# Optimization experiments

Hardware: AMD Instinct MI355X
Metric: run time of the kernel (lower is better)

Reference implementation:

```python
import jax, jax.numpy as jnp
import numpy as np

B, C, H, W = 16, 1024, 64, 64  # H*W must equal 64*64=4096 per module math
KDIM = 64

def setup_inputs() -> dict:
    key = jax.random.key(0)
    k1, k2 = jax.random.split(key)
    x = jax.random.normal(k1, (B, C, H, W), dtype=jnp.float32)
    martx = jax.random.normal(k2, (1, H * W, KDIM), dtype=jnp.float32) * 0.02
    aphal = jnp.ones((1,), dtype=jnp.float32)
    gamma = jnp.ones((1,), dtype=jnp.float32)
    return {"x": x, "martx": martx, "aphal": aphal, "gamma": gamma}

def reference(x, martx, aphal, gamma):
    b, c, h, w = x.shape
    n = h * w  # 4096
    q = x.reshape(b, c, n)                      # proj_query: (B, C, N)
    kbank = martx[0]                            # (N, 64), shared across batch
    # energy = bmm(q, martx): (B, C, 64)
    energy = jnp.einsum('bcn,nk->bck', q, kbank)
    # inverted max-subtract trick, then scaled softmax over last dim
    energy_new = jnp.max(energy, axis=-1, keepdims=True) - energy
    attention = jax.nn.softmax(aphal[0] * energy_new, axis=-1)  # (B, C, 64)
    # out = bmm(attention, martx^T): (B, C, N)
    out = jnp.einsum('bck,nk->bcn', attention, kbank)
    out = out.reshape(b, c, h, w)
    return gamma[0] * out + x
```

## Files before the change

kernel.cpp:

```cpp
#include <hip/hip_runtime.h>
#include <hip/hip_bf16.h>


using frag_ab = __attribute__((ext_vector_type(8))) short;
using f32x4   = __attribute__((ext_vector_type(4))) float;

#define MFMA16(a, b, c) __builtin_amdgcn_mfma_f32_16x16x32_bf16((a), (b), (c), 0, 0, 0)

static __device__ __forceinline__ unsigned short f2bf_bits(float f) {
    __hip_bfloat16 h = __float2bfloat16(f);
    return *reinterpret_cast<const unsigned short*>(&h);
}
static __device__ __forceinline__ float bf2f(unsigned short u) {
    return __uint_as_float(((unsigned)u) << 16);
}
static __device__ __forceinline__ frag_ab load_frag(const __hip_bfloat16* p) {
    return *reinterpret_cast<const frag_ab*>(p);
}
static __device__ __forceinline__ frag_ab cvt2(float4 a, float4 b) {
    frag_ab r;
    r[0] = (short)f2bf_bits(a.x); r[1] = (short)f2bf_bits(a.y);
    r[2] = (short)f2bf_bits(a.z); r[3] = (short)f2bf_bits(a.w);
    r[4] = (short)f2bf_bits(b.x); r[5] = (short)f2bf_bits(b.y);
    r[6] = (short)f2bf_bits(b.z); r[7] = (short)f2bf_bits(b.w);
    return r;
}

__global__ __launch_bounds__(256) void prep_frags(
        const float* __restrict__ M,
        __hip_bfloat16* __restrict__ MtF, __hip_bfloat16* __restrict__ MbfF) {
    const int w    = threadIdx.x >> 6;
    const int lane = threadIdx.x & 63;
    const int g    = lane >> 4;
    const int r15  = lane & 15;
    const int f    = blockIdx.x * 4 + w;
    if (f < 512) {
        const int slot = f >> 2, t = f & 3;
        frag_ab fr;
#pragma unroll
        for (int j = 0; j < 8; ++j)
            fr[j] = (short)f2bf_bits(M[(size_t)(32 * slot + 8 * g + j) * 64 + 16 * t + r15]);
        *reinterpret_cast<frag_ab*>(MtF + ((size_t)f * 64 + lane) * 8) = fr;
    } else {
        const int f2 = f - 512;
        const float* src = M + (size_t)(16 * (f2 >> 1) + r15) * 64 + 32 * (f2 & 1) + 8 * g;
        float4 a = *reinterpret_cast<const float4*>(src);
        float4 b = *reinterpret_cast<const float4*>(src + 4);
        *reinterpret_cast<frag_ab*>(MbfF + ((size_t)f2 * 64 + lane) * 8) = cvt2(a, b);
    }
}

__global__ __launch_bounds__(1024, 1) void ccam_fused(
        const float* __restrict__ x,
        const __hip_bfloat16* __restrict__ MtF,
        const __hip_bfloat16* __restrict__ MbfF,
        const float* __restrict__ aphal,
        const float* __restrict__ gamma,
        float* __restrict__ out) {
    __shared__ __align__(16) char smem[147712];
    float* Ep = (float*)(smem + 131328);

    const int tid  = threadIdx.x;
    const int w    = tid >> 6;
    const int lane = tid & 63;
    const int g    = lane >> 4;
    const int r15  = lane & 15;
    const int rowbase = blockIdx.x * 16;

    const float alpha = aphal[0];
    const float gam   = gamma[0];

    {
        const float* xr = x + (size_t)(rowbase + w) * 4096;
        char* dst = smem + w * 8208;
#pragma unroll
        for (int rnd = 0; rnd < 2; ++rnd) {
            f32x4 v[8];
#pragma unroll
            for (int i = 0; i < 8; ++i)
                v[i] = __builtin_nontemporal_load(
                    reinterpret_cast<const f32x4*>(xr + rnd * 2048 + i * 256 + 4 * lane));
#pragma unroll
            for (int i = 0; i < 8; ++i) {
                ushort4 u;
                u.x = f2bf_bits(v[i][0]); u.y = f2bf_bits(v[i][1]);
                u.z = f2bf_bits(v[i][2]); u.w = f2bf_bits(v[i][3]);
                *reinterpret_cast<ushort4*>(dst + (rnd * 2048 + i * 256 + 4 * lane) * 2) = u;
            }
        }
    }
    __syncthreads();

    const int t1 = w >> 2;
    const int kq = w & 3;
    {
        f32x4 acc = {0.f, 0.f, 0.f, 0.f};
        const char* arow = smem + r15 * 8208;
        const int kbase = kq * 1024;
        const int slot0 = kq * 32;
        frag_ab Bc = load_frag(MtF + (((size_t)slot0 * 4 + t1) * 64 + lane) * 8);
        frag_ab Bn = load_frag(MtF + (((size_t)(slot0 + 1) * 4 + t1) * 64 + lane) * 8);
#pragma unroll 4
        for (int s = 0; s < 32; ++s) {
            frag_ab Bn2 = Bn;
            if (s < 30)
                Bn2 = load_frag(MtF + (((size_t)(slot0 + s + 2) * 4 + t1) * 64 + lane) * 8);
            frag_ab A = *reinterpret_cast<const frag_ab*>(
                arow + (kbase + 32 * s + 8 * g) * 2);
            acc = MFMA16(A, Bc, acc);
            Bc = Bn;
            Bn = Bn2;
        }
#pragma unroll
        for (int reg = 0; reg < 4; ++reg)
            Ep[(((t1 * 4 + kq) * 16) + 4 * g + reg) * 16 + r15] = acc[reg];
    }
    __syncthreads();

    float elo[8], ehi[8];
    {
        const int t0  = g >> 1;
        const int off = 8 * (g & 1);
#pragma unroll
        for (int j = 0; j < 8; ++j) { elo[j] = 0.f; ehi[j] = 0.f; }
#pragma unroll
        for (int q = 0; q < 4; ++q) {
            const float* pl = Ep + ((t0 * 4 + q) * 16 + r15) * 16 + off;
            const float* ph = Ep + (((t0 + 2) * 4 + q) * 16 + r15) * 16 + off;
            float4 a0 = *reinterpret_cast<const float4*>(pl);
            float4 a1 = *reinterpret_cast<const float4*>(pl + 4);
            elo[0] += a0.x; elo[1] += a0.y; elo[2] += a0.z; elo[3] += a0.w;
            elo[4] += a1.x; elo[5] += a1.y; elo[6] += a1.z; elo[7] += a1.w;
            float4 c0 = *reinterpret_cast<const float4*>(ph);
            float4 c1 = *reinterpret_cast<const float4*>(ph + 4);
            ehi[0] += c0.x; ehi[1] += c0.y; ehi[2] += c0.z; ehi[3] += c0.w;
            ehi[4] += c1.x; ehi[5] += c1.y; ehi[6] += c1.z; ehi[7] += c1.w;
        }
    }
    float m = elo[0];
#pragma unroll
    for (int j = 1; j < 8; ++j) m = fmaxf(m, elo[j]);
#pragma unroll
    for (int j = 0; j < 8; ++j) m = fmaxf(m, ehi[j]);
    m = fmaxf(m, __shfl_xor(m, 16, 64));
    m = fmaxf(m, __shfl_xor(m, 32, 64));
#pragma unroll
    for (int j = 0; j < 8; ++j) { elo[j] = alpha * (m - elo[j]); ehi[j] = alpha * (m - ehi[j]); }
    float vm = elo[0];
#pragma unroll
    for (int j = 1; j < 8; ++j) vm = fmaxf(vm, elo[j]);
#pragma unroll
    for (int j = 0; j < 8; ++j) vm = fmaxf(vm, ehi[j]);
    vm = fmaxf(vm, __shfl_xor(vm, 16, 64));
    vm = fmaxf(vm, __shfl_xor(vm, 32, 64));
    float s = 0.f;
#pragma unroll
    for (int j = 0; j < 8; ++j) { elo[j] = __expf(elo[j] - vm); s += elo[j]; }
#pragma unroll
    for (int j = 0; j < 8; ++j) { ehi[j] = __expf(ehi[j] - vm); s += ehi[j]; }
    s += __shfl_xor(s, 16, 64);
    s += __shfl_xor(s, 32, 64);
    const float sc = gam / s;
    frag_ab A0, A1;
#pragma unroll
    for (int j = 0; j < 8; ++j) {
        A0[j] = (short)f2bf_bits(elo[j] * sc);
        A1[j] = (short)f2bf_bits(ehi[j] * sc);
    }

#pragma unroll 1
    for (int gi = 0; gi < 4; ++gi) {
        const int grp = 4 * w + gi;
        frag_ab B[4][2];
#pragma unroll
        for (int t = 0; t < 4; ++t)
#pragma unroll
            for (int h = 0; h < 2; ++h)
                B[t][h] = load_frag(MbfF + (((size_t)(4 * grp + t) * 2 + h) * 64 + lane) * 8);
        f32x4 d0 = {0.f, 0.f, 0.f, 0.f};
        f32x4 d1 = d0, d2 = d0, d3 = d0;
        d0 = MFMA16(A0, B[0][0], d0); d0 = MFMA16(A1, B[0][1], d0);
        d1 = MFMA16(A0, B[1][0], d1); d1 = MFMA16(A1, B[1][1], d1);
        d2 = MFMA16(A0, B[2][0], d2); d2 = MFMA16(A1, B[2][1], d2);
        d3 = MFMA16(A0, B[3][0], d3); d3 = MFMA16(A1, B[3][1], d3);
        const int colbase = grp * 64 + r15;
#pragma unroll
        for (int reg = 0; reg < 4; ++reg) {
            unsigned short* p =
                (unsigned short*)(smem + (4 * g + reg) * 8208) + colbase;
            p[ 0] = f2bf_bits(d0[reg] + bf2f(p[ 0]));
            p[16] = f2bf_bits(d1[reg] + bf2f(p[16]));
            p[32] = f2bf_bits(d2[reg] + bf2f(p[32]));
            p[48] = f2bf_bits(d3[reg] + bf2f(p[48]));
        }
    }
    __syncthreads();

    {
        const char* srow = smem + w * 8208;
        float* orow = out + (size_t)(rowbase + w) * 4096;
#pragma unroll
        for (int i = 0; i < 16; ++i) {
            const int col = 256 * i + 4 * lane;
            ushort4 u = *reinterpret_cast<const ushort4*>(srow + col * 2);
            f32x4 v;
            v[0] = bf2f(u.x); v[1] = bf2f(u.y); v[2] = bf2f(u.z); v[3] = bf2f(u.w);
            __builtin_nontemporal_store(v, reinterpret_cast<f32x4*>(orow + col));
        }
    }
}

extern "C" void kernel_launch(void* const* d_in, const int* in_sizes, int n_in,
                              void* d_out, int out_size, void* d_ws, size_t ws_size,
                              hipStream_t stream) {
    const float* x     = (const float*)d_in[0];
    const float* M     = (const float*)d_in[1];
    const float* aphal = (const float*)d_in[2];
    const float* gamma = (const float*)d_in[3];
    __hip_bfloat16* MtF  = (__hip_bfloat16*)d_ws;
    __hip_bfloat16* MbfF = (__hip_bfloat16*)d_ws + 64 * 4096;

    hipLaunchKernelGGL(prep_frags, dim3(256), dim3(256), 0, stream, M, MtF, MbfF);
    hipLaunchKernelGGL(ccam_fused, dim3(1024), dim3(1024), 0, stream,
                       x, MtF, MbfF, aphal, gamma, (float*)d_out);
}
```

Before: 126.5 us.

## Make fused kernel persistent with column-owned store and next-tile prefetch

The grid shrinks from 1024 to 256 blocks, and each block loops over four 16-row tiles. Every wave owns a 256-column slice, so after the second GEMM it writes its output columns and loads the next tile's x columns into the same LDS slice without an extra barrier. This removes per-block launch and ramp cost and keeps the two LDS barriers per tile. The risk is less overlap between blocks, since each CU now runs a single long-lived block whose phases are serialized.

```diff
diff --git a/kernel.cpp b/kernel.cpp
--- a/kernel.cpp
+++ b/kernel.cpp
@@ -65,13 +65,16 @@
     const int lane = tid & 63;
     const int g    = lane >> 4;
     const int r15  = lane & 15;
-    const int rowbase = blockIdx.x * 16;
 
     const float alpha = aphal[0];
     const float gam   = gamma[0];
 
+    const int t1 = w >> 2;
+    const int kq = w & 3;
+    const int cb = 256 * w;
+
     {
-        const float* xr = x + (size_t)(rowbase + w) * 4096;
+        const float* xr = x + ((size_t)blockIdx.x * 16 + w) * 4096;
         char* dst = smem + w * 8208;
 #pragma unroll
         for (int rnd = 0; rnd < 2; ++rnd) {
@@ -91,122 +94,133 @@
     }
     __syncthreads();
 
-    const int t1 = w >> 2;
-    const int kq = w & 3;
-    {
-        f32x4 acc = {0.f, 0.f, 0.f, 0.f};
-        const char* arow = smem + r15 * 8208;
-        const int kbase = kq * 1024;
-        const int slot0 = kq * 32;
-        frag_ab Bc = load_frag(MtF + (((size_t)slot0 * 4 + t1) * 64 + lane) * 8);
-        frag_ab Bn = load_frag(MtF + (((size_t)(slot0 + 1) * 4 + t1) * 64 + lane) * 8);
+#pragma unroll 1
+    for (int gen = 0; gen < 4; ++gen) {
+        const int rowbase = (blockIdx.x + 256 * gen) * 16;
+
+        {
+            f32x4 acc = {0.f, 0.f, 0.f, 0.f};
+            const char* arow = smem + r15 * 8208;
+            const int kbase = kq * 1024;
+            const int slot0 = kq * 32;
+            frag_ab Bc = load_frag(MtF + (((size_t)slot0 * 4 + t1) * 64 + lane) * 8);
+            frag_ab Bn = load_frag(MtF + (((size_t)(slot0 + 1) * 4 + t1) * 64 + lane) * 8);
 #pragma unroll 4
-        for (int s = 0; s < 32; ++s) {
-            frag_ab Bn2 = Bn;
-            if (s < 30)
-                Bn2 = load_frag(MtF + (((size_t)(slot0 + s + 2) * 4 + t1) * 64 + lane) * 8);
-            frag_ab A = *reinterpret_cast<const frag_ab*>(
-                arow + (kbase + 32 * s + 8 * g) * 2);
-            acc = MFMA16(A, Bc, acc);
-            Bc = Bn;
-            Bn = Bn2;
-        }
-#pragma unroll
-        for (int reg = 0; reg < 4; ++reg)
-            Ep[(((t1 * 4 + kq) * 16) + 4 * g + reg) * 16 + r15] = acc[reg];
-    }
-    __syncthreads();
-
-    float elo[8], ehi[8];
-    {
-        const int t0  = g >> 1;
-        const int off = 8 * (g & 1);
-#pragma unroll
-        for (int j = 0; j < 8; ++j) { elo[j] = 0.f; ehi[j] = 0.f; }
-#pragma unroll
-        for (int q = 0; q < 4; ++q) {
-            const float* pl = Ep + ((t0 * 4 + q) * 16 + r15) * 16 + off;
-            const float* ph = Ep + (((t0 + 2) * 4 + q) * 16 + r15) * 16 + off;
-            float4 a0 = *reinterpret_cast<const float4*>(pl);
-            float4 a1 = *reinterpret_cast<const float4*>(pl + 4);
-            elo[0] += a0.x; elo[1] += a0.y; elo[2] += a0.z; elo[3] += a0.w;
-            elo[4] += a1.x; elo[5] += a1.y; elo[6] += a1.z; elo[7] += a1.w;
-            float4 c0 = *reinterpret_cast<const float4*>(ph);
-            float4 c1 = *reinterpret_cast<const float4*>(ph + 4);
-            ehi[0] += c0.x; ehi[1] += c0.y; ehi[2] += c0.z; ehi[3] += c0.w;
-            ehi[4] += c1.x; ehi[5] += c1.y; ehi[6] += c1.z; ehi[7] += c1.w;
-        }
-    }
-    float m = elo[0];
-#pragma unroll
-    for (int j = 1; j < 8; ++j) m = fmaxf(m, elo[j]);
-#pragma unroll
-    for (int j = 0; j < 8; ++j) m = fmaxf(m, ehi[j]);
-    m = fmaxf(m, __shfl_xor(m, 16, 64));
-    m = fmaxf(m, __shfl_xor(m, 32, 64));
-#pragma unroll
-    for (int j = 0; j < 8; ++j) { elo[j] = alpha * (m - elo[j]); ehi[j] = alpha * (m - ehi[j]); }
-    float vm = elo[0];
-#pragma unroll
-    for (int j = 1; j < 8; ++j) vm = fmaxf(vm, elo[j]);
-#pragma unroll
-    for (int j = 0; j < 8; ++j) vm = fmaxf(vm, ehi[j]);
-    vm = fmaxf(vm, __shfl_xor(vm, 16, 64));
-    vm = fmaxf(vm, __shfl_xor(vm, 32, 64));
-    float s = 0.f;
-#pragma unroll
-    for (int j = 0; j < 8; ++j) { elo[j] = __expf(elo[j] - vm); s += elo[j]; }
-#pragma unroll
-    for (int j = 0; j < 8; ++j) { ehi[j] = __expf(ehi[j] - vm); s += ehi[j]; }
-    s += __shfl_xor(s, 16, 64);
-    s += __shfl_xor(s, 32, 64);
-    const float sc = gam / s;
-    frag_ab A0, A1;
-#pragma unroll
-    for (int j = 0; j < 8; ++j) {
-        A0[j] = (short)f2bf_bits(elo[j] * sc);
-        A1[j] = (short)f2bf_bits(ehi[j] * sc);
-    }
+            for (int s = 0; s < 32; ++s) {
+                frag_ab Bn2 = Bn;
+                if (s < 30)
+                    Bn2 = load_frag(MtF + (((size_t)(slot0 + s + 2) * 4 + t1) * 64 + lane) * 8);
+                frag_ab A = *reinterpret_cast<const frag_ab*>(
+                    arow + (kbase + 32 * s + 8 * g) * 2);
+                acc = MFMA16(A, Bc, acc);
+                Bc = Bn;
+                Bn = Bn2;
+            }
+#pragma unroll
+            for (int reg = 0; reg < 4; ++reg)
+                Ep[(((t1 * 4 + kq) * 16) + 4 * g + reg) * 16 + r15] = acc[reg];
+        }
+        __syncthreads();
+
+        float elo[8], ehi[8];
+        {
+            const int t0  = g >> 1;
+            const int off = 8 * (g & 1);
+#pragma unroll
+            for (int j = 0; j < 8; ++j) { elo[j] = 0.f; ehi[j] = 0.f; }
+#pragma unroll
+            for (int q = 0; q < 4; ++q) {
+                const float* pl = Ep + ((t0 * 4 + q) * 16 + r15) * 16 + off;
+                const float* ph = Ep + (((t0 + 2) * 4 + q) * 16 + r15) * 16 + off;
+                float4 a0 = *reinterpret_cast<const float4*>(pl);
+                float4 a1 = *reinterpret_cast<const float4*>(pl + 4);
+                elo[0] += a0.x; elo[1] += a0.y; elo[2] += a0.z; elo[3] += a0.w;
+                elo[4] += a1.x; elo[5] += a1.y; elo[6] += a1.z; elo[7] += a1.w;
+                float4 c0 = *reinterpret_cast<const float4*>(ph);
+                float4 c1 = *reinterpret_cast<const float4*>(ph + 4);
+                ehi[0] += c0.x; ehi[1] += c0.y; ehi[2] += c0.z; ehi[3] += c0.w;
+                ehi[4] += c1.x; ehi[5] += c1.y; ehi[6] += c1.z; ehi[7] += c1.w;
+            }
+        }
+        float m = elo[0];
+#pragma unroll
+        for (int j = 1; j < 8; ++j) m = fmaxf(m, elo[j]);
+#pragma unroll
+        for (int j = 0; j < 8; ++j) m = fmaxf(m, ehi[j]);
+        m = fmaxf(m, __shfl_xor(m, 16, 64));
+        m = fmaxf(m, __shfl_xor(m, 32, 64));
+#pragma unroll
+        for (int j = 0; j < 8; ++j) { elo[j] = alpha * (m - elo[j]); ehi[j] = alpha * (m - ehi[j]); }
+        float vm = elo[0];
+#pragma unroll
+        for (int j = 1; j < 8; ++j) vm = fmaxf(vm, elo[j]);
+#pragma unroll
+        for (int j = 0; j < 8; ++j) vm = fmaxf(vm, ehi[j]);
+        vm = fmaxf(vm, __shfl_xor(vm, 16, 64));
+        vm = fmaxf(vm, __shfl_xor(vm, 32, 64));
+        float s = 0.f;
+#pragma unroll
+        for (int j = 0; j < 8; ++j) { elo[j] = __expf(elo[j] - vm); s += elo[j]; }
+#pragma unroll
+        for (int j = 0; j < 8; ++j) { ehi[j] = __expf(ehi[j] - vm); s += ehi[j]; }
+        s += __shfl_xor(s, 16, 64);
+        s += __shfl_xor(s, 32, 64);
+        const float sc = gam / s;
+        frag_ab A0, A1;
+#pragma unroll
+        for (int j = 0; j < 8; ++j) {
+            A0[j] = (short)f2bf_bits(elo[j] * sc);
+            A1[j] = (short)f2bf_bits(ehi[j] * sc);
+        }
 
 #pragma unroll 1
-    for (int gi = 0; gi < 4; ++gi) {
-        const int grp = 4 * w + gi;
-        frag_ab B[4][2];
-#pragma unroll
-        for (int t = 0; t < 4; ++t)
-#pragma unroll
-            for (int h = 0; h < 2; ++h)
-                B[t][h] = load_frag(MbfF + (((size_t)(4 * grp + t) * 2 + h) * 64 + lane) * 8);
-        f32x4 d0 = {0.f, 0.f, 0.f, 0.f};
-        f32x4 d1 = d0, d2 = d0, d3 = d0;
-        d0 = MFMA16(A0, B[0][0], d0); d0 = MFMA16(A1, B[0][1], d0);
-        d1 = MFMA16(A0, B[1][0], d1); d1 = MFMA16(A1, B[1][1], d1);
-        d2 = MFMA16(A0, B[2][0], d2); d2 = MFMA16(A1, B[2][1], d2);
-        d3 = MFMA16(A0, B[3][0], d3); d3 = MFMA16(A1, B[3][1], d3);
-        const int colbase = grp * 64 + r15;
-#pragma unroll
-        for (int reg = 0; reg < 4; ++reg) {
-            unsigned short* p =
-                (unsigned short*)(smem + (4 * g + reg) * 8208) + colbase;
-            p[ 0] = f2bf_bits(d0[reg] + bf2f(p[ 0]));
-            p[16] = f2bf_bits(d1[reg] + bf2f(p[16]));
-            p[32] = f2bf_bits(d2[reg] + bf2f(p[32]));
-            p[48] = f2bf_bits(d3[reg] + bf2f(p[48]));
-        }
-    }
-    __syncthreads();
-
-    {
-        const char* srow = smem + w * 8208;
-        float* orow = out + (size_t)(rowbase + w) * 4096;
-#pragma unroll
-        for (int i = 0; i < 16; ++i) {
-            const int col = 256 * i + 4 * lane;
-            ushort4 u = *reinterpret_cast<const ushort4*>(srow + col * 2);
+        for (int gi = 0; gi < 4; ++gi) {
+            const int grp = 4 * w + gi;
+            frag_ab B[4][2];
+#pragma unroll
+            for (int t = 0; t < 4; ++t)
+#pragma unroll
+                for (int h = 0; h < 2; ++h)
+                    B[t][h] = load_frag(MbfF + (((size_t)(4 * grp + t) * 2 + h) * 64 + lane) * 8);
+            f32x4 d0 = {0.f, 0.f, 0.f, 0.f};
+            f32x4 d1 = d0, d2 = d0, d3 = d0;
+            d0 = MFMA16(A0, B[0][0], d0); d0 = MFMA16(A1, B[0][1], d0);
+            d1 = MFMA16(A0, B[1][0], d1); d1 = MFMA16(A1, B[1][1], d1);
+            d2 = MFMA16(A0, B[2][0], d2); d2 = MFMA16(A1, B[2][1], d2);
+            d3 = MFMA16(A0, B[3][0], d3); d3 = MFMA16(A1, B[3][1], d3);
+            const int colbase = grp * 64 + r15;
+#pragma unroll
+            for (int reg = 0; reg < 4; ++reg) {
+                unsigned short* p =
+                    (unsigned short*)(smem + (4 * g + reg) * 8208) + colbase;
+                p[ 0] = f2bf_bits(d0[reg] + bf2f(p[ 0]));
+                p[16] = f2bf_bits(d1[reg] + bf2f(p[16]));
+                p[32] = f2bf_bits(d2[reg] + bf2f(p[32]));
+                p[48] = f2bf_bits(d3[reg] + bf2f(p[48]));
+            }
+        }
+#pragma unroll
+        for (int r = 0; r < 16; ++r) {
+            const char* srow = smem + r * 8208;
+            ushort4 u = *reinterpret_cast<const ushort4*>(srow + (cb + 4 * lane) * 2);
             f32x4 v;
             v[0] = bf2f(u.x); v[1] = bf2f(u.y); v[2] = bf2f(u.z); v[3] = bf2f(u.w);
-            __builtin_nontemporal_store(v, reinterpret_cast<f32x4*>(orow + col));
-        }
+            __builtin_nontemporal_store(
+                v, reinterpret_cast<f32x4*>(out + (size_t)(rowbase + r) * 4096 + cb + 4 * lane));
+        }
+        if (gen < 3) {
+            const int rownext = (blockIdx.x + 256 * (gen + 1)) * 16;
+#pragma unroll
+            for (int r = 0; r < 16; ++r) {
+                f32x4 v = __builtin_nontemporal_load(
+                    reinterpret_cast<const f32x4*>(x + (size_t)(rownext + r) * 4096 + cb + 4 * lane));
+                ushort4 u;
+                u.x = f2bf_bits(v[0]); u.y = f2bf_bits(v[1]);
+                u.z = f2bf_bits(v[2]); u.w = f2bf_bits(v[3]);
+                *reinterpret_cast<ushort4*>(smem + r * 8208 + (cb + 4 * lane) * 2) = u;
+            }
+        }
+        __syncthreads();
     }
 }
 
@@ -221,6 +235,6 @@
     __hip_bfloat16* MbfF = (__hip_bfloat16*)d_ws + 64 * 4096;
 
     hipLaunchKernelGGL(prep_frags, dim3(256), dim3(256), 0, stream, M, MtF, MbfF);
-    hipLaunchKernelGGL(ccam_fused, dim3(1024), dim3(1024), 0, stream,
+    hipLaunchKernelGGL(ccam_fused, dim3(256), dim3(1024), 0, stream,
                        x, MtF, MbfF, aphal, gamma, (float*)d_out);
 }
```

Result: slower. 129.7 us (+2.5%).

## Pipeline x row loading in quarters overlapped with energy MFMA stage

Applied to the files above, without the earlier changes.

Splits the load of each x row into four 1024-column chunks and overlaps the global load of the next chunk with the MFMA energy computation on the already-staged chunk. Waves whose k-quarter matches the current chunk compute while all waves prefetch the next chunk. This hides global memory latency behind the first GEMM, but it serializes the MFMA work so only a quarter of the waves compute at a time, and it adds three extra block-wide barriers.

```diff
diff --git a/kernel.cpp b/kernel.cpp
--- a/kernel.cpp
+++ b/kernel.cpp
@@ -70,52 +70,78 @@
     const float alpha = aphal[0];
     const float gam   = gamma[0];
 
+    const int t1 = w >> 2;
+    const int kq = w & 3;
+    const int slot0 = kq * 32;
+
+    frag_ab Bc = load_frag(MtF + (((size_t)slot0 * 4 + t1) * 64 + lane) * 8);
+    frag_ab Bn = load_frag(MtF + (((size_t)(slot0 + 1) * 4 + t1) * 64 + lane) * 8);
+
     {
         const float* xr = x + (size_t)(rowbase + w) * 4096;
         char* dst = smem + w * 8208;
-#pragma unroll
-        for (int rnd = 0; rnd < 2; ++rnd) {
-            f32x4 v[8];
-#pragma unroll
-            for (int i = 0; i < 8; ++i)
-                v[i] = __builtin_nontemporal_load(
-                    reinterpret_cast<const f32x4*>(xr + rnd * 2048 + i * 256 + 4 * lane));
-#pragma unroll
-            for (int i = 0; i < 8; ++i) {
-                ushort4 u;
-                u.x = f2bf_bits(v[i][0]); u.y = f2bf_bits(v[i][1]);
-                u.z = f2bf_bits(v[i][2]); u.w = f2bf_bits(v[i][3]);
-                *reinterpret_cast<ushort4*>(dst + (rnd * 2048 + i * 256 + 4 * lane) * 2) = u;
+        f32x4 v[4];
+#pragma unroll
+        for (int i = 0; i < 4; ++i)
+            v[i] = __builtin_nontemporal_load(
+                reinterpret_cast<const f32x4*>(xr + i * 256 + 4 * lane));
+#pragma unroll
+        for (int i = 0; i < 4; ++i) {
+            ushort4 u;
+            u.x = f2bf_bits(v[i][0]); u.y = f2bf_bits(v[i][1]);
+            u.z = f2bf_bits(v[i][2]); u.w = f2bf_bits(v[i][3]);
+            *reinterpret_cast<ushort4*>(dst + (i * 256 + 4 * lane) * 2) = u;
+        }
+    }
+    __syncthreads();
+
+#pragma unroll
+    for (int q = 0; q < 4; ++q) {
+        f32x4 v0, v1, v2, v3;
+        if (q < 3) {
+            const float* xr = x + (size_t)(rowbase + w) * 4096 + (q + 1) * 1024;
+            v0 = __builtin_nontemporal_load(reinterpret_cast<const f32x4*>(xr + 0 * 256 + 4 * lane));
+            v1 = __builtin_nontemporal_load(reinterpret_cast<const f32x4*>(xr + 1 * 256 + 4 * lane));
+            v2 = __builtin_nontemporal_load(reinterpret_cast<const f32x4*>(xr + 2 * 256 + 4 * lane));
+            v3 = __builtin_nontemporal_load(reinterpret_cast<const f32x4*>(xr + 3 * 256 + 4 * lane));
+        }
+        if (kq == q) {
+            f32x4 acc = {0.f, 0.f, 0.f, 0.f};
+            const char* arow = smem + r15 * 8208;
+            const int kbase = kq * 1024;
+#pragma unroll 4
+            for (int s = 0; s < 32; ++s) {
+                frag_ab Bn2 = Bn;
+                if (s < 30)
+                    Bn2 = load_frag(MtF + (((size_t)(slot0 + s + 2) * 4 + t1) * 64 + lane) * 8);
+                frag_ab A = *reinterpret_cast<const frag_ab*>(
+                    arow + (kbase + 32 * s + 8 * g) * 2);
+                acc = MFMA16(A, Bc, acc);
+                Bc = Bn;
+                Bn = Bn2;
             }
-        }
-    }
-    __syncthreads();
-
-    const int t1 = w >> 2;
-    const int kq = w & 3;
-    {
-        f32x4 acc = {0.f, 0.f, 0.f, 0.f};
-        const char* arow = smem + r15 * 8208;
-        const int kbase = kq * 1024;
-        const int slot0 = kq * 32;
-        frag_ab Bc = load_frag(MtF + (((size_t)slot0 * 4 + t1) * 64 + lane) * 8);
-        frag_ab Bn = load_frag(MtF + (((size_t)(slot0 + 1) * 4 + t1) * 64 + lane) * 8);
-#pragma unroll 4
-        for (int s = 0; s < 32; ++s) {
-            frag_ab Bn2 = Bn;
-            if (s < 30)
-                Bn2 = load_frag(MtF + (((size_t)(slot0 + s + 2) * 4 + t1) * 64 + lane) * 8);
-            frag_ab A = *reinterpret_cast<const frag_ab*>(
-                arow + (kbase + 32 * s + 8 * g) * 2);
-            acc = MFMA16(A, Bc, acc);
-            Bc = Bn;
-            Bn = Bn2;
-        }
-#pragma unroll
-        for (int reg = 0; reg < 4; ++reg)
-            Ep[(((t1 * 4 + kq) * 16) + 4 * g + reg) * 16 + r15] = acc[reg];
-    }
-    __syncthreads();
+#pragma unroll
+            for (int reg = 0; reg < 4; ++reg)
+                Ep[(((t1 * 4 + kq) * 16) + 4 * g + reg) * 16 + r15] = acc[reg];
+        }
+        if (q < 3) {
+            char* dst = smem + w * 8208 + (q + 1) * 2048;
+            ushort4 u;
+            u.x = f2bf_bits(v0[0]); u.y = f2bf_bits(v0[1]);
+            u.z = f2bf_bits(v0[2]); u.w = f2bf_bits(v0[3]);
+            *reinterpret_cast<ushort4*>(dst + (0 * 256 + 4 * lane) * 2) = u;
+            u.x = f2bf_bits(v1[0]); u.y = f2bf_bits(v1[1]);
+            u.z = f2bf_bits(v1[2]); u.w = f2bf_bits(v1[3]);
+            *reinterpret_cast<ushort4*>(dst + (1 * 256 + 4 * lane) * 2) = u;
+            u.x = f2bf_bits(v2[0]); u.y = f2bf_bits(v2[1]);
+            u.z = f2bf_bits(v2[2]); u.w = f2bf_bits(v2[3]);
+            *reinterpret_cast<ushort4*>(dst + (2 * 256 + 4 * lane) * 2) = u;
+            u.x = f2bf_bits(v3[0]); u.y = f2bf_bits(v3[1]);
+            u.z = f2bf_bits(v3[2]); u.w = f2bf_bits(v3[3]);
+            *reinterpret_cast<ushort4*>(dst + (3 * 256 + 4 * lane) * 2) = u;
+        }
+        __syncthreads();
+    }
 
     float elo[8], ehi[8];
     {
```

Result: slower. 159.0 us (+25.7%).
